# Kernel optimization log

Hardware: AMD Instinct MI355X
Metric: run time of the kernel (lower is better)

Reference implementation:

```python
import jax, jax.numpy as jnp
import numpy as np

D, T, B = 128, 64, 512
EPS = 1e-5


def setup_inputs() -> dict:
    key = jax.random.key(0)
    k1, k2, k3, k4, k5 = jax.random.split(key, 5)
    inp = jax.random.normal(k1, (D, T, B), jnp.float32) * 0.1
    returns_partition = jax.random.normal(k2, (D, T, B), jnp.float32) * 0.01
    target = jax.random.normal(k3, (D,), jnp.float32) * 0.1
    hidden = jnp.zeros((D, 1, B), jnp.float32)  # forward arg (overwritten at t=0)
    # diagonally-dominant weight so the per-row denominators v[j,j] stay away from 0
    W = jnp.eye(D, dtype=jnp.float32) + 0.1 * jax.random.normal(k4, (D, D), jnp.float32)
    b = 0.1 * jax.random.normal(k5, (D,), jnp.float32)
    return {"input": inp, "target": target, "returns_partition": returns_partition,
            "hidden": hidden, "W": W, "b": b}


def _recurrence(h, v, absb, pi_bar):
    # h, pi_bar: [D, B]; v: [D, D] (row-normalized); absb: [D]
    d = h.shape[0]
    vd = jnp.diagonal(v)                                  # v[j, j], torch.matmul(vj, e_j)
    s = v @ (h - pi_bar)                                  # [D, B], s[j] = vj . (h - pi_bar)
    lam_p = (absb[:, None] - s) / vd[:, None]
    lam_m = (-absb[:, None] - s) / vd[:, None]
    delta = (jnp.where(s > absb[:, None], lam_p, 0.0)
             + jnp.where(s < -absb[:, None], lam_m, 0.0))  # [D, B]
    # hidden_new_j = h + delta[j] * e_j  =>  v @ (hidden_new_j - pi_bar) = s + v[:, j] (x) delta[j]
    snew = s[None, :, :] + v.T[:, :, None] * delta[:, None, :]      # [J, D, B]
    inside = (snew < absb[None, :, None] + EPS) & (snew > -absb[None, :, None] - EPS)
    # torch: judge_mat[j] = min over rows; then max over j  == any_j(all_k(...))
    judge_mat = jnp.any(jnp.all(inside, axis=1), axis=0).astype(h.dtype)  # [B]

    # sequential per-coordinate projection (order matters: row j uses updated state)
    def body(ht, j):
        sj = v[j] @ (ht - pi_bar)                          # [B]
        lp = (absb[j] - sj) / v[j, j]
        lm = (-absb[j] - sj) / v[j, j]
        dj = jnp.where(sj > absb[j], lp, 0.0) + jnp.where(sj < -absb[j], lm, 0.0)
        return ht.at[j].add(dj), None
    h_temp, _ = jax.lax.scan(body, h, jnp.arange(d))

    # 10-step bisection between pi_bar (feasible) and (1 - judge_mat) * h
    def bis(carry, _):
        h_in, h_out = carry
        h_m = h_in + (h_out - h_in) * 0.5
        sm = v @ (h_m - pi_bar)
        j = jnp.all((sm <= absb[:, None] + EPS) & (sm >= -absb[:, None] - EPS), axis=0)  # [B]
        return (jnp.where(j, h_m, h_in), jnp.where(j, h_out, h_m)), h_m
    h_out0 = (1.0 - judge_mat) * h
    _, h_ms = jax.lax.scan(bis, (pi_bar, h_out0), None, length=10)
    h_m = h_ms[-1]
    return judge_mat * h_temp + (1.0 - judge_mat) * h_m


def reference(input, target, returns_partition, hidden, W, b):
    d, t, bsz = input.shape
    norm = jnp.linalg.norm(W, axis=1, keepdims=True)
    v = W / jnp.maximum(norm, 1e-12)                      # F.normalize(W, p=2, dim=1)
    absb = jnp.abs(b)
    pi_bar = jnp.broadcast_to(target[:, None], (d, bsz))  # [D, B]

    h0 = input[:, 0, :]                                   # t = 0: hidden := input slice
    rs = jnp.moveaxis(returns_partition[:, :t - 1, :], 1, 0)  # [T-1, D, B]

    def step(h, r):
        adj = h * (1.0 + r) / (1.0 + jnp.sum(h * r, axis=0))
        hn = _recurrence(adj, v, absb, pi_bar)
        return hn, hn

    h_last, hs = jax.lax.scan(step, h0, rs)
    output = jnp.concatenate([h0[:, None, :], jnp.moveaxis(hs, 0, 1)], axis=1)  # [D, T, B]
    return output, h_last[:, None, :]
```

## Files before the change

kernel.cpp:

```cpp
#include <hip/hip_runtime.h>
#include <cstdint>

#define D 128
#define T 64
#define B 512
#define EPSF 1e-5f

__device__ __forceinline__ float lane_bcast(float x, int l) {
    return __int_as_float(__builtin_amdgcn_readlane(__float_as_int(x), l));
}

__global__ __launch_bounds__(64) void prep_kernel(const float* __restrict__ W,
                                                  const float* __restrict__ b,
                                                  float* __restrict__ vT,
                                                  float* __restrict__ vd,
                                                  float* __restrict__ absb) {
    const int i = blockIdx.x;
    const int l = threadIdx.x;
    float w0 = W[i * D + l];
    float w1 = W[i * D + l + 64];
    float p = w0 * w0 + w1 * w1;
#pragma unroll
    for (int off = 32; off; off >>= 1) p += __shfl_xor(p, off);
    float norm = sqrtf(p);
    float scale = norm > 1e-12f ? norm : 1e-12f;
    float v0 = w0 / scale;
    float v1 = w1 / scale;
    vT[l * D + i] = v0;
    vT[(l + 64) * D + i] = v1;
    if (i < 64) {
        if (l == i) vd[i] = v0;
    } else {
        if (l == i - 64) vd[i] = v1;
    }
    if (i == 0) {
        absb[l] = fabsf(b[l]);
        absb[l + 64] = fabsf(b[l + 64]);
    }
}

__global__ __launch_bounds__(128) void rnn_kernel(const float* __restrict__ input,
                                                  const float* __restrict__ target,
                                                  const float* __restrict__ returns,
                                                  const float* __restrict__ vTg,
                                                  const float* __restrict__ vdg,
                                                  const float* __restrict__ absbg,
                                                  float* __restrict__ out) {
    __shared__ float vsh[D * D];

    const int tid = threadIdx.x;
    {
        const float4* src = (const float4*)vTg;
        float4* dst = (float4*)vsh;
#pragma unroll
        for (int c = 0; c < 32; ++c) {
            int f = c * 128 + tid;
            int k = f >> 5;
            int i = (f & 31) << 2;
            int ck = (k & 7) << 2;
            int d4 = k * 32 + (((i ^ ck)) >> 2);
            dst[d4] = src[f];
        }
    }
    __syncthreads();

    const int w = tid >> 6;
    const int lane = tid & 63;
    const int b = blockIdx.x * 2 + w;
    const int rlo = lane, rhi = lane + 64;

    const float tgt_lo = target[rlo], tgt_hi = target[rhi];
    const float a_lo = absbg[rlo], a_hi = absbg[rhi];
    const float aeps_lo = a_lo + EPSF, aeps_hi = a_hi + EPSF;
    const float vd_lo = vdg[rlo], vd_hi = vdg[rhi];
    const float rvd_lo = 1.0f / vd_lo, rvd_hi = 1.0f / vd_hi;

    int ax[8];
#pragma unroll
    for (int c = 0; c < 8; ++c) ax[c] = rlo ^ (c << 2);

    const int cj = (lane & 7) << 2;
    int Abase[8];
#pragma unroll
    for (int c = 0; c < 8; ++c) Abase[c] = lane * 128 + ((c << 2) ^ cj);

    float h_lo = input[rlo * T * B + b];
    float h_hi = input[rhi * T * B + b];
    out[rlo * T * B + b] = h_lo;
    out[rhi * T * B + b] = h_hi;

    float r_lo = returns[rlo * T * B + b];
    float r_hi = returns[rhi * T * B + b];

    for (int t = 1; t < T; ++t) {
        float num_lo = h_lo * (1.0f + r_lo);
        float num_hi = h_hi * (1.0f + r_hi);
        float p = h_lo * r_lo + h_hi * r_hi;
#pragma unroll
        for (int off = 32; off; off >>= 1) p += __shfl_xor(p, off);
        float den = 1.0f + p;
        float adj_lo = num_lo / den;
        float adj_hi = num_hi / den;

        if (t < T - 1) {
            r_lo = returns[rlo * T * B + t * B + b];
            r_hi = returns[rhi * T * B + t * B + b];
        }

        const float x_lo = adj_lo - tgt_lo;
        const float x_hi = adj_hi - tgt_hi;

        float s_lo = 0.0f, s_hi = 0.0f;
#pragma unroll
        for (int k = 0; k < 64; ++k) {
            float xb = lane_bcast(x_lo, k);
            s_lo = fmaf(vsh[k * 128 + ax[k & 7]], xb, s_lo);
            s_hi = fmaf(vsh[k * 128 + ax[k & 7] + 64], xb, s_hi);
        }
#pragma unroll
        for (int k = 0; k < 64; ++k) {
            float xb = lane_bcast(x_hi, k);
            s_lo = fmaf(vsh[(k + 64) * 128 + ax[k & 7]], xb, s_lo);
            s_hi = fmaf(vsh[(k + 64) * 128 + ax[k & 7] + 64], xb, s_hi);
        }

        h_lo = adj_lo;
        h_hi = adj_hi;

        bool viol_lo = (s_lo > a_lo) || (s_lo < -a_lo);
        bool viol_hi = (s_hi > a_hi) || (s_hi < -a_hi);
        uint64_t mlo = __ballot(viol_lo);
        uint64_t mhi = __ballot(viol_hi);

        if ((mlo | mhi) != 0ull) {
            float dl = 0.0f, dh = 0.0f;
            if (s_lo > a_lo) dl = (a_lo - s_lo) / vd_lo;
            else if (s_lo < -a_lo) dl = (-a_lo - s_lo) / vd_lo;
            if (s_hi > a_hi) dh = (a_hi - s_hi) / vd_hi;
            else if (s_hi < -a_hi) dh = (-a_hi - s_hi) / vd_hi;

            int V = __popcll(mlo) + __popcll(mhi);
            bool judge;

            if (V <= 8) {
                bool in_lo = (s_lo < aeps_lo) && (s_lo > -aeps_lo);
                bool in_hi = (s_hi < aeps_hi) && (s_hi > -aeps_hi);
                judge = (__ballot(in_lo && in_hi) == ~0ull);
                if (!judge) {
                    uint64_t t_mlo = mlo, t_mhi = mhi;
                    while (t_mlo | t_mhi) {
                        int j;
                        float dj;
                        if (t_mlo) {
                            int jl = (int)__ffsll((unsigned long long)t_mlo) - 1;
                            t_mlo &= t_mlo - 1;
                            j = jl;
                            dj = lane_bcast(dl, jl);
                        } else {
                            int jh = (int)__ffsll((unsigned long long)t_mhi) - 1;
                            t_mhi &= t_mhi - 1;
                            j = 64 + jh;
                            dj = lane_bcast(dh, jh);
                        }
                        int cjj = (j & 7) << 2;
                        int base = j * 128 + (rlo ^ cjj);
                        float n_lo = fmaf(vsh[base], dj, s_lo);
                        float n_hi = fmaf(vsh[base + 64], dj, s_hi);
                        bool pl = (n_lo < aeps_lo) && (n_lo > -aeps_lo);
                        bool ph = (n_hi < aeps_hi) && (n_hi > -aeps_hi);
                        if (__ballot(pl && ph) == ~0ull) { judge = true; break; }
                    }
                }
            } else {
                float m1 = -1.0f, m2 = -1.0f;
#pragma unroll
                for (int a = 0; a < 4; ++a) {
#pragma unroll
                    for (int c = 0; c < 8; ++c) {
                        const int i0 = a * 32 + c * 4;
                        const float* p1 = &vsh[Abase[c] + 32 * a];
                        float4 c1 = *(const float4*)p1;
                        float4 c2 = *(const float4*)(p1 + 8192);
#pragma unroll
                        for (int e = 0; e < 4; ++e) {
                            const int i = i0 + e;
                            float sv = (i < 64) ? lane_bcast(s_lo, i)
                                                : lane_bcast(s_hi, i - 64);
                            float ae = (i < 64) ? lane_bcast(aeps_lo, i)
                                                : lane_bcast(aeps_hi, i - 64);
                            float f1 = ((const float*)&c1)[e];
                            float f2 = ((const float*)&c2)[e];
                            m1 = fmaxf(m1, fabsf(fmaf(f1, dl, sv)) - ae);
                            m2 = fmaxf(m2, fabsf(fmaf(f2, dh, sv)) - ae);
                        }
                    }
                }
                judge = ((__ballot(m1 < 0.0f) | __ballot(m2 < 0.0f)) != 0ull);
            }

            if (judge) {
                uint64_t rem_lo = ~0ull, rem_hi = ~0ull;
                while (true) {
                    uint64_t m1b = __ballot((s_lo > a_lo) || (s_lo < -a_lo)) & rem_lo;
                    uint64_t m2b = __ballot((s_hi > a_hi) || (s_hi < -a_hi)) & rem_hi;
                    int j;
                    if (m1b) {
                        int jl = (int)__ffsll((unsigned long long)m1b) - 1;
                        j = jl;
                        rem_lo = (jl == 63) ? 0ull : (~0ull << (jl + 1));
                    } else if (m2b) {
                        int jh = (int)__ffsll((unsigned long long)m2b) - 1;
                        j = 64 + jh;
                        rem_lo = 0ull;
                        rem_hi = (jh == 63) ? 0ull : (~0ull << (jh + 1));
                    } else {
                        break;
                    }
                    float dl2 = (s_lo > a_lo) ? (a_lo - s_lo) * rvd_lo
                               : ((s_lo < -a_lo) ? (-a_lo - s_lo) * rvd_lo : 0.0f);
                    float dh2 = (s_hi > a_hi) ? (a_hi - s_hi) * rvd_hi
                               : ((s_hi < -a_hi) ? (-a_hi - s_hi) * rvd_hi : 0.0f);
                    float srcv = (j < 64) ? dl2 : dh2;
                    float dj = lane_bcast(srcv, j & 63);
                    if (lane == (j & 63)) {
                        if (j < 64) h_lo += dj; else h_hi += dj;
                    }
                    int cjj = (j & 7) << 2;
                    int base = j * 128 + (rlo ^ cjj);
                    s_lo = fmaf(vsh[base], dj, s_lo);
                    s_hi = fmaf(vsh[base + 64], dj, s_hi);
                }
            } else {
                float hin_lo = tgt_lo, hin_hi = tgt_hi;
                float sin_lo = 0.0f, sin_hi = 0.0f;
                float hout_lo = h_lo, hout_hi = h_hi;
                float sout_lo = s_lo, sout_hi = s_hi;
                float hm_lo = 0.0f, hm_hi = 0.0f;
#pragma unroll
                for (int it = 0; it < 10; ++it) {
                    hm_lo = hin_lo + (hout_lo - hin_lo) * 0.5f;
                    hm_hi = hin_hi + (hout_hi - hin_hi) * 0.5f;
                    float sm_lo = sin_lo + (sout_lo - sin_lo) * 0.5f;
                    float sm_hi = sin_hi + (sout_hi - sin_hi) * 0.5f;
                    bool pl = (sm_lo <= aeps_lo) && (sm_lo >= -aeps_lo);
                    bool ph = (sm_hi <= aeps_hi) && (sm_hi >= -aeps_hi);
                    bool inside = (__ballot(pl && ph) == ~0ull);
                    if (inside) {
                        hin_lo = hm_lo; hin_hi = hm_hi;
                        sin_lo = sm_lo; sin_hi = sm_hi;
                    } else {
                        hout_lo = hm_lo; hout_hi = hm_hi;
                        sout_lo = sm_lo; sout_hi = sm_hi;
                    }
                }
                h_lo = hm_lo;
                h_hi = hm_hi;
            }
        }

        out[rlo * T * B + t * B + b] = h_lo;
        out[rhi * T * B + t * B + b] = h_hi;
    }

    out[D * T * B + rlo * B + b] = h_lo;
    out[D * T * B + rhi * B + b] = h_hi;
}

extern "C" void kernel_launch(void* const* d_in, const int* in_sizes, int n_in,
                              void* d_out, int out_size, void* d_ws, size_t ws_size,
                              hipStream_t stream) {
    const float* input   = (const float*)d_in[0];
    const float* target  = (const float*)d_in[1];
    const float* returns = (const float*)d_in[2];
    const float* W = (const float*)d_in[4];
    const float* b = (const float*)d_in[5];
    float* out = (float*)d_out;

    float* vT   = (float*)d_ws;
    float* vd   = vT + D * D;
    float* absb = vd + D;

    prep_kernel<<<D, 64, 0, stream>>>(W, b, vT, vd, absb);
    rnn_kernel<<<B / 2, 128, 0, stream>>>(input, target, returns, vT, vd, absb, out);
}
```

Measured before the change: 217.6 us.

## Keep normalized W rows in registers for the matvec and restructure LDS layouts

```diff
diff --git a/kernel.cpp b/kernel.cpp
--- a/kernel.cpp
+++ b/kernel.cpp
@@ -10,9 +10,14 @@
     return __int_as_float(__builtin_amdgcn_readlane(__float_as_int(x), l));
 }
 
+__device__ __forceinline__ float2 colpair(const float* csh, int j, int i2) {
+    int f2 = j * 64 + (i2 ^ ((j & 7) << 1));
+    return *(const float2*)(csh + 2 * f2);
+}
+
 __global__ __launch_bounds__(64) void prep_kernel(const float* __restrict__ W,
                                                   const float* __restrict__ b,
-                                                  float* __restrict__ vT,
+                                                  float* __restrict__ csw,
                                                   float* __restrict__ vd,
                                                   float* __restrict__ absb) {
     const int i = blockIdx.x;
@@ -26,48 +31,42 @@
     float scale = norm > 1e-12f ? norm : 1e-12f;
     float v0 = w0 / scale;
     float v1 = w1 / scale;
-    vT[l * D + i] = v0;
-    vT[(l + 64) * D + i] = v1;
-    if (i < 64) {
-        if (l == i) vd[i] = v0;
-    } else {
-        if (l == i - 64) vd[i] = v1;
-    }
+    const int i2 = i & 63, half = i >> 6;
+    const int sw = (l & 7) << 1;
+    csw[2 * (l * 64 + (i2 ^ sw)) + half] = v0;
+    csw[2 * ((l + 64) * 64 + (i2 ^ sw)) + half] = v1;
+    if (i < 64) { if (l == i) vd[i] = v0; }
+    else        { if (l == i - 64) vd[i] = v1; }
     if (i == 0) {
         absb[l] = fabsf(b[l]);
         absb[l + 64] = fabsf(b[l + 64]);
     }
 }
 
-__global__ __launch_bounds__(128) void rnn_kernel(const float* __restrict__ input,
-                                                  const float* __restrict__ target,
-                                                  const float* __restrict__ returns,
-                                                  const float* __restrict__ vTg,
-                                                  const float* __restrict__ vdg,
-                                                  const float* __restrict__ absbg,
-                                                  float* __restrict__ out) {
-    __shared__ float vsh[D * D];
+__global__ __launch_bounds__(128, 1) void rnn_kernel(const float* __restrict__ input,
+                                                     const float* __restrict__ target,
+                                                     const float* __restrict__ returns,
+                                                     const float* __restrict__ W,
+                                                     const float* __restrict__ cswg,
+                                                     const float* __restrict__ vdg,
+                                                     const float* __restrict__ absbg,
+                                                     float* __restrict__ out) {
+    __shared__ float csh[D * D];
+    __shared__ float s_sh[2][2 * 64];
+    __shared__ float ae_sh[2 * 64];
 
     const int tid = threadIdx.x;
-    {
-        const float4* src = (const float4*)vTg;
-        float4* dst = (float4*)vsh;
-#pragma unroll
-        for (int c = 0; c < 32; ++c) {
-            int f = c * 128 + tid;
-            int k = f >> 5;
-            int i = (f & 31) << 2;
-            int ck = (k & 7) << 2;
-            int d4 = k * 32 + (((i ^ ck)) >> 2);
-            dst[d4] = src[f];
-        }
-    }
-    __syncthreads();
-
     const int w = tid >> 6;
     const int lane = tid & 63;
     const int b = blockIdx.x * 2 + w;
     const int rlo = lane, rhi = lane + 64;
+
+    {
+        const float4* src = (const float4*)cswg;
+        float4* dst = (float4*)csh;
+#pragma unroll
+        for (int c = 0; c < 32; ++c) dst[c * 128 + tid] = src[c * 128 + tid];
+    }
 
     const float tgt_lo = target[rlo], tgt_hi = target[rhi];
     const float a_lo = absbg[rlo], a_hi = absbg[rhi];
@@ -75,14 +74,37 @@
     const float vd_lo = vdg[rlo], vd_hi = vdg[rhi];
     const float rvd_lo = 1.0f / vd_lo, rvd_hi = 1.0f / vd_hi;
 
-    int ax[8];
-#pragma unroll
-    for (int c = 0; c < 8; ++c) ax[c] = rlo ^ (c << 2);
-
-    const int cj = (lane & 7) << 2;
-    int Abase[8];
-#pragma unroll
-    for (int c = 0; c < 8; ++c) Abase[c] = lane * 128 + ((c << 2) ^ cj);
+    if (w == 0) *(float2*)&ae_sh[2 * lane] = make_float2(aeps_lo, aeps_hi);
+
+    float4 va4[32], vb4[32];
+    {
+        const float4* wa = (const float4*)(W + rlo * D);
+        const float4* wb = (const float4*)(W + rhi * D);
+        float na0 = 0, na1 = 0, na2 = 0, na3 = 0;
+        float nb0 = 0, nb1 = 0, nb2 = 0, nb3 = 0;
+#pragma unroll
+        for (int c = 0; c < 32; ++c) {
+            float4 A = wa[c], Bv = wb[c];
+            va4[c] = A; vb4[c] = Bv;
+            na0 = fmaf(A.x, A.x, na0); na1 = fmaf(A.y, A.y, na1);
+            na2 = fmaf(A.z, A.z, na2); na3 = fmaf(A.w, A.w, na3);
+            nb0 = fmaf(Bv.x, Bv.x, nb0); nb1 = fmaf(Bv.y, Bv.y, nb1);
+            nb2 = fmaf(Bv.z, Bv.z, nb2); nb3 = fmaf(Bv.w, Bv.w, nb3);
+        }
+        float nna = sqrtf((na0 + na1) + (na2 + na3));
+        float nnb = sqrtf((nb0 + nb1) + (nb2 + nb3));
+        float ra = 1.0f / (nna > 1e-12f ? nna : 1e-12f);
+        float rb = 1.0f / (nnb > 1e-12f ? nnb : 1e-12f);
+#pragma unroll
+        for (int c = 0; c < 32; ++c) {
+            va4[c].x *= ra; va4[c].y *= ra; va4[c].z *= ra; va4[c].w *= ra;
+            vb4[c].x *= rb; vb4[c].y *= rb; vb4[c].z *= rb; vb4[c].w *= rb;
+        }
+    }
+    __syncthreads();
+
+    const float* va = (const float*)va4;
+    const float* vb = (const float*)vb4;
 
     float h_lo = input[rlo * T * B + b];
     float h_hi = input[rhi * T * B + b];
@@ -110,19 +132,20 @@
         const float x_lo = adj_lo - tgt_lo;
         const float x_hi = adj_hi - tgt_hi;
 
-        float s_lo = 0.0f, s_hi = 0.0f;
-#pragma unroll
-        for (int k = 0; k < 64; ++k) {
-            float xb = lane_bcast(x_lo, k);
-            s_lo = fmaf(vsh[k * 128 + ax[k & 7]], xb, s_lo);
-            s_hi = fmaf(vsh[k * 128 + ax[k & 7] + 64], xb, s_hi);
-        }
-#pragma unroll
-        for (int k = 0; k < 64; ++k) {
-            float xb = lane_bcast(x_hi, k);
-            s_lo = fmaf(vsh[(k + 64) * 128 + ax[k & 7]], xb, s_lo);
-            s_hi = fmaf(vsh[(k + 64) * 128 + ax[k & 7] + 64], xb, s_hi);
-        }
+        float a0 = 0, a1 = 0, a2 = 0, a3 = 0;
+        float b0 = 0, b1 = 0, b2 = 0, b3 = 0;
+#pragma unroll
+        for (int k = 0; k < 128; ++k) {
+            float xk = (k < 64) ? lane_bcast(x_lo, k) : lane_bcast(x_hi, k - 64);
+            switch (k & 3) {
+                case 0: a0 = fmaf(va[k], xk, a0); b0 = fmaf(vb[k], xk, b0); break;
+                case 1: a1 = fmaf(va[k], xk, a1); b1 = fmaf(vb[k], xk, b1); break;
+                case 2: a2 = fmaf(va[k], xk, a2); b2 = fmaf(vb[k], xk, b2); break;
+                default: a3 = fmaf(va[k], xk, a3); b3 = fmaf(vb[k], xk, b3); break;
+            }
+        }
+        float s_lo = (a0 + a1) + (a2 + a3);
+        float s_hi = (b0 + b1) + (b2 + b3);
 
         h_lo = adj_lo;
         h_hi = adj_hi;
@@ -140,60 +163,62 @@
             else if (s_hi < -a_hi) dh = (-a_hi - s_hi) / vd_hi;
 
             int V = __popcll(mlo) + __popcll(mhi);
-            bool judge;
+            bool judge = false;
 
             if (V <= 8) {
                 bool in_lo = (s_lo < aeps_lo) && (s_lo > -aeps_lo);
                 bool in_hi = (s_hi < aeps_hi) && (s_hi > -aeps_hi);
                 judge = (__ballot(in_lo && in_hi) == ~0ull);
                 if (!judge) {
-                    uint64_t t_mlo = mlo, t_mhi = mhi;
-                    while (t_mlo | t_mhi) {
-                        int j;
-                        float dj;
-                        if (t_mlo) {
-                            int jl = (int)__ffsll((unsigned long long)t_mlo) - 1;
-                            t_mlo &= t_mlo - 1;
-                            j = jl;
-                            dj = lane_bcast(dl, jl);
-                        } else {
-                            int jh = (int)__ffsll((unsigned long long)t_mhi) - 1;
-                            t_mhi &= t_mhi - 1;
-                            j = 64 + jh;
-                            dj = lane_bcast(dh, jh);
+                    uint64_t tml = mlo, tmh = mhi;
+                    int jn[8];
+                    float djs[8];
+                    float2 cps[8];
+#pragma unroll
+                    for (int q = 0; q < 8; ++q) {
+                        int j = -1;
+                        if (tml) {
+                            j = (int)__ffsll((unsigned long long)tml) - 1;
+                            tml &= tml - 1;
+                        } else if (tmh) {
+                            j = 64 + (int)__ffsll((unsigned long long)tmh) - 1;
+                            tmh &= tmh - 1;
                         }
-                        int cjj = (j & 7) << 2;
-                        int base = j * 128 + (rlo ^ cjj);
-                        float n_lo = fmaf(vsh[base], dj, s_lo);
-                        float n_hi = fmaf(vsh[base + 64], dj, s_hi);
-                        bool pl = (n_lo < aeps_lo) && (n_lo > -aeps_lo);
-                        bool ph = (n_hi < aeps_hi) && (n_hi > -aeps_hi);
-                        if (__ballot(pl && ph) == ~0ull) { judge = true; break; }
+                        jn[q] = j;
+                        if (j >= 0) {
+                            djs[q] = lane_bcast((j < 64) ? dl : dh, j & 63);
+                            cps[q] = colpair(csh, j, lane);
+                        }
+                    }
+#pragma unroll
+                    for (int q = 0; q < 8; ++q) {
+                        if (jn[q] >= 0 && !judge) {
+                            float n_lo = fmaf(cps[q].x, djs[q], s_lo);
+                            float n_hi = fmaf(cps[q].y, djs[q], s_hi);
+                            bool pl = (n_lo < aeps_lo) && (n_lo > -aeps_lo);
+                            bool ph = (n_hi < aeps_hi) && (n_hi > -aeps_hi);
+                            if (__ballot(pl && ph) == ~0ull) judge = true;
+                        }
                     }
                 }
             } else {
+                *(float2*)&s_sh[w][2 * lane] = make_float2(s_lo, s_hi);
                 float m1 = -1.0f, m2 = -1.0f;
 #pragma unroll
-                for (int a = 0; a < 4; ++a) {
-#pragma unroll
-                    for (int c = 0; c < 8; ++c) {
-                        const int i0 = a * 32 + c * 4;
-                        const float* p1 = &vsh[Abase[c] + 32 * a];
-                        float4 c1 = *(const float4*)p1;
-                        float4 c2 = *(const float4*)(p1 + 8192);
-#pragma unroll
-                        for (int e = 0; e < 4; ++e) {
-                            const int i = i0 + e;
-                            float sv = (i < 64) ? lane_bcast(s_lo, i)
-                                                : lane_bcast(s_hi, i - 64);
-                            float ae = (i < 64) ? lane_bcast(aeps_lo, i)
-                                                : lane_bcast(aeps_hi, i - 64);
-                            float f1 = ((const float*)&c1)[e];
-                            float f2 = ((const float*)&c2)[e];
-                            m1 = fmaxf(m1, fabsf(fmaf(f1, dl, sv)) - ae);
-                            m2 = fmaxf(m2, fabsf(fmaf(f2, dh, sv)) - ae);
-                        }
-                    }
+                for (int c = 0; c < 32; ++c) {
+                    int f4 = lane * 32 + (c ^ (lane & 7));
+                    float4 c1 = *(const float4*)(csh + 4 * f4);
+                    float4 c2 = *(const float4*)(csh + 4 * f4 + 8192);
+                    float4 sv = *(const float4*)&s_sh[w][4 * c];
+                    float4 ae = *(const float4*)&ae_sh[4 * c];
+                    m1 = fmaxf(m1, fabsf(fmaf(c1.x, dl, sv.x)) - ae.x);
+                    m1 = fmaxf(m1, fabsf(fmaf(c1.y, dl, sv.y)) - ae.y);
+                    m1 = fmaxf(m1, fabsf(fmaf(c1.z, dl, sv.z)) - ae.z);
+                    m1 = fmaxf(m1, fabsf(fmaf(c1.w, dl, sv.w)) - ae.w);
+                    m2 = fmaxf(m2, fabsf(fmaf(c2.x, dh, sv.x)) - ae.x);
+                    m2 = fmaxf(m2, fabsf(fmaf(c2.y, dh, sv.y)) - ae.y);
+                    m2 = fmaxf(m2, fabsf(fmaf(c2.z, dh, sv.z)) - ae.z);
+                    m2 = fmaxf(m2, fabsf(fmaf(c2.w, dh, sv.w)) - ae.w);
                 }
                 judge = ((__ballot(m1 < 0.0f) | __ballot(m2 < 0.0f)) != 0ull);
             }
@@ -225,10 +250,9 @@
                     if (lane == (j & 63)) {
                         if (j < 64) h_lo += dj; else h_hi += dj;
                     }
-                    int cjj = (j & 7) << 2;
-                    int base = j * 128 + (rlo ^ cjj);
-                    s_lo = fmaf(vsh[base], dj, s_lo);
-                    s_hi = fmaf(vsh[base + 64], dj, s_hi);
+                    float2 cp = colpair(csh, j, lane);
+                    s_lo = fmaf(cp.x, dj, s_lo);
+                    s_hi = fmaf(cp.y, dj, s_hi);
                 }
             } else {
                 float hin_lo = tgt_lo, hin_hi = tgt_hi;
@@ -276,10 +300,10 @@
     const float* b = (const float*)d_in[5];
     float* out = (float*)d_out;
 
-    float* vT   = (float*)d_ws;
-    float* vd   = vT + D * D;
+    float* csw  = (float*)d_ws;
+    float* vd   = csw + D * D;
     float* absb = vd + D;
 
-    prep_kernel<<<D, 64, 0, stream>>>(W, b, vT, vd, absb);
-    rnn_kernel<<<B / 2, 128, 0, stream>>>(input, target, returns, vT, vd, absb, out);
-}
+    prep_kernel<<<D, 64, 0, stream>>>(W, b, csw, vd, absb);
+    rnn_kernel<<<B / 2, 128, 0, stream>>>(input, target, returns, W, csw, vd, absb, out);
+}
```

Result: slower. 239.5 us (+10.0%).

## Restructure matvec with LDS-staged x and float4 v reads, batch sparse judge loads

Applied to the files above, without the earlier changes.

```diff
diff --git a/kernel.cpp b/kernel.cpp
--- a/kernel.cpp
+++ b/kernel.cpp
@@ -47,6 +47,8 @@
                                                   const float* __restrict__ absbg,
                                                   float* __restrict__ out) {
     __shared__ float vsh[D * D];
+    __shared__ __align__(16) float xs[2][128];
+    __shared__ __align__(16) float ss[2][128];
 
     const int tid = threadIdx.x;
     {
@@ -75,9 +77,11 @@
     const float vd_lo = vdg[rlo], vd_hi = vdg[rhi];
     const float rvd_lo = 1.0f / vd_lo, rvd_hi = 1.0f / vd_hi;
 
-    int ax[8];
-#pragma unroll
-    for (int c = 0; c < 8; ++c) ax[c] = rlo ^ (c << 2);
+    const int m = lane & 31, u = lane >> 5;
+    const char* vq[8];
+#pragma unroll
+    for (int c = 0; c < 8; ++c)
+        vq[c] = (const char*)vsh + 16 * (m ^ c) + u * 32768;
 
     const int cj = (lane & 7) << 2;
     int Abase[8];
@@ -98,9 +102,9 @@
         float p = h_lo * r_lo + h_hi * r_hi;
 #pragma unroll
         for (int off = 32; off; off >>= 1) p += __shfl_xor(p, off);
-        float den = 1.0f + p;
-        float adj_lo = num_lo / den;
-        float adj_hi = num_hi / den;
+        float rden = 1.0f / (1.0f + p);
+        float adj_lo = num_lo * rden;
+        float adj_hi = num_hi * rden;
 
         if (t < T - 1) {
             r_lo = returns[rlo * T * B + t * B + b];
@@ -110,19 +114,30 @@
         const float x_lo = adj_lo - tgt_lo;
         const float x_hi = adj_hi - tgt_hi;
 
-        float s_lo = 0.0f, s_hi = 0.0f;
-#pragma unroll
-        for (int k = 0; k < 64; ++k) {
-            float xb = lane_bcast(x_lo, k);
-            s_lo = fmaf(vsh[k * 128 + ax[k & 7]], xb, s_lo);
-            s_hi = fmaf(vsh[k * 128 + ax[k & 7] + 64], xb, s_hi);
+        xs[w][lane] = x_lo;
+        xs[w][64 + lane] = x_hi;
+        float ac0 = 0, ac1 = 0, ac2 = 0, ac3 = 0;
+#pragma unroll
+        for (int q = 0; q < 16; ++q) {
+            float4 x4 = *(const float4*)&xs[w][64 * u + 4 * q];
+#pragma unroll
+            for (int e = 0; e < 4; ++e) {
+                const int kk = 4 * q + e;
+                float4 vv = *(const float4*)(vq[kk & 7] + kk * 512);
+                float xe = (&x4.x)[e];
+                ac0 = fmaf(vv.x, xe, ac0);
+                ac1 = fmaf(vv.y, xe, ac1);
+                ac2 = fmaf(vv.z, xe, ac2);
+                ac3 = fmaf(vv.w, xe, ac3);
+            }
         }
-#pragma unroll
-        for (int k = 0; k < 64; ++k) {
-            float xb = lane_bcast(x_hi, k);
-            s_lo = fmaf(vsh[(k + 64) * 128 + ax[k & 7]], xb, s_lo);
-            s_hi = fmaf(vsh[(k + 64) * 128 + ax[k & 7] + 64], xb, s_hi);
-        }
+        ac0 += __shfl_xor(ac0, 32);
+        ac1 += __shfl_xor(ac1, 32);
+        ac2 += __shfl_xor(ac2, 32);
+        ac3 += __shfl_xor(ac3, 32);
+        if (u == 0) *(float4*)&ss[w][4 * m] = make_float4(ac0, ac1, ac2, ac3);
+        float s_lo = ss[w][lane];
+        float s_hi = ss[w][64 + lane];
 
         h_lo = adj_lo;
         h_hi = adj_hi;
@@ -140,35 +155,44 @@
             else if (s_hi < -a_hi) dh = (-a_hi - s_hi) / vd_hi;
 
             int V = __popcll(mlo) + __popcll(mhi);
-            bool judge;
+            bool judge = false;
 
             if (V <= 8) {
                 bool in_lo = (s_lo < aeps_lo) && (s_lo > -aeps_lo);
                 bool in_hi = (s_hi < aeps_hi) && (s_hi > -aeps_hi);
                 judge = (__ballot(in_lo && in_hi) == ~0ull);
                 if (!judge) {
-                    uint64_t t_mlo = mlo, t_mhi = mhi;
-                    while (t_mlo | t_mhi) {
-                        int j;
-                        float dj;
-                        if (t_mlo) {
-                            int jl = (int)__ffsll((unsigned long long)t_mlo) - 1;
-                            t_mlo &= t_mlo - 1;
-                            j = jl;
-                            dj = lane_bcast(dl, jl);
-                        } else {
-                            int jh = (int)__ffsll((unsigned long long)t_mhi) - 1;
-                            t_mhi &= t_mhi - 1;
-                            j = 64 + jh;
-                            dj = lane_bcast(dh, jh);
+                    uint64_t tml = mlo, tmh = mhi;
+                    int jn[8];
+                    float djs[8];
+                    float2 cps[8];
+#pragma unroll
+                    for (int q = 0; q < 8; ++q) {
+                        int j = -1;
+                        if (tml) {
+                            j = (int)__ffsll((unsigned long long)tml) - 1;
+                            tml &= tml - 1;
+                        } else if (tmh) {
+                            j = 64 + (int)__ffsll((unsigned long long)tmh) - 1;
+                            tmh &= tmh - 1;
                         }
-                        int cjj = (j & 7) << 2;
-                        int base = j * 128 + (rlo ^ cjj);
-                        float n_lo = fmaf(vsh[base], dj, s_lo);
-                        float n_hi = fmaf(vsh[base + 64], dj, s_hi);
-                        bool pl = (n_lo < aeps_lo) && (n_lo > -aeps_lo);
-                        bool ph = (n_hi < aeps_hi) && (n_hi > -aeps_hi);
-                        if (__ballot(pl && ph) == ~0ull) { judge = true; break; }
+                        jn[q] = j;
+                        if (j >= 0) {
+                            djs[q] = lane_bcast((j < 64) ? dl : dh, j & 63);
+                            int cjj = (j & 7) << 2;
+                            int base = j * 128 + (rlo ^ cjj);
+                            cps[q] = make_float2(vsh[base], vsh[base + 64]);
+                        }
+                    }
+#pragma unroll
+                    for (int q = 0; q < 8; ++q) {
+                        if (jn[q] >= 0 && !judge) {
+                            float n_lo = fmaf(cps[q].x, djs[q], s_lo);
+                            float n_hi = fmaf(cps[q].y, djs[q], s_hi);
+                            bool pl = (n_lo < aeps_lo) && (n_lo > -aeps_lo);
+                            bool ph = (n_hi < aeps_hi) && (n_hi > -aeps_hi);
+                            if (__ballot(pl && ph) == ~0ull) judge = true;
+                        }
                     }
                 }
             } else {
```

After: 259.0 us. 19.0% more time.
